# Kernel optimization log

Hardware: AMD Instinct MI355X
Metric: run time of the kernel (lower is better)

## Reference

```python
import jax, jax.numpy as jnp
from jax import lax
import numpy as np

# Layer configuration (from init_kwargs; see FilteringActLayer.__init__)
UP = 2                      # up_factor (temp_rate 32 / in_rate 16)
DOWN = 2                    # down_factor (temp_rate 32 / out_rate 16)
PADDING = (11, 10, 11, 10)  # (px0, px1, py0, py1), derived pad_total = 21
GAIN = float(np.sqrt(2.0))  # lrelu gain used in StyleGAN3
SLOPE = 0.2                 # leaky relu negative slope
CLAMP = 256.0               # activation clamp
UP_TAPS = 12
IN_CUTOFF = 8.0
OUT_CUTOFF = 8.0
IN_HALF_WIDTH = 6.0
OUT_HALF_WIDTH = 6.0
TEMP_FS = 32.0              # max(in_rate, out_rate) * act_upsampling


def _design_lowpass(numtaps, cutoff, width, fs):
    """Replicates scipy.signal.firwin(numtaps, cutoff, width=width, fs=fs)."""
    nyq = fs / 2.0
    # kaiser_atten / kaiser_beta
    atten = 2.285 * (numtaps - 1) * np.pi * (width / nyq) + 7.95
    if atten > 50.0:
        beta = 0.1102 * (atten - 8.7)
    elif atten > 21.0:
        beta = 0.5842 * (atten - 21.0) ** 0.4 + 0.07886 * (atten - 21.0)
    else:
        beta = 0.0
    m = np.arange(numtaps) - (numtaps - 1) / 2.0
    c = cutoff / nyq
    h = c * np.sinc(c * m)
    h = h * np.kaiser(numtaps, beta)
    h = h / np.sum(h)  # unity gain at DC (firwin scale=True)
    return h.astype(np.float32)


def _upfirdn2d_sep(x, f, up, down, pad, gain):
    """Zero-insert upsample by `up`, pad, correlate with separable 1D FIR f
    (applied flipped, i.e. true convolution as in the torch reference),
    then subsample by `down`. x: [N,C,H,W], f: [taps]."""
    N, C, H, W = x.shape
    fr = f[::-1].astype(x.dtype)
    kH = fr.reshape(1, 1, -1, 1)
    kW = fr.reshape(1, 1, 1, -1)
    px0, px1, py0, py1 = pad
    xr = x.reshape(N * C, 1, H, W)
    # lhs_dilation implements the zero-insertion; +up-1 hi-pad accounts for the
    # trailing zeros the torch reference keeps after upsampling.
    xr = lax.conv_general_dilated(xr, kH, window_strides=(down, 1),
                                  padding=((py0, py1 + up - 1), (0, 0)),
                                  lhs_dilation=(up, 1))
    xr = lax.conv_general_dilated(xr, kW, window_strides=(1, down),
                                  padding=((0, 0), (px0, px1 + up - 1)),
                                  lhs_dilation=(1, up))
    Ho, Wo = xr.shape[2], xr.shape[3]
    return xr.reshape(N, C, Ho, Wo) * gain


def setup_inputs() -> dict:
    key = jax.random.key(0)
    k1, k2 = jax.random.split(key)
    x = jax.random.normal(k1, (8, 512, 64, 64), dtype=jnp.float32)
    bias = jax.random.normal(k2, (512,), dtype=jnp.float32) * 0.1
    up_filter = jnp.asarray(_design_lowpass(UP_TAPS, IN_CUTOFF, IN_HALF_WIDTH * 2, TEMP_FS))
    down_filter = jnp.asarray(_design_lowpass(UP_TAPS, OUT_CUTOFF, OUT_HALF_WIDTH * 2, TEMP_FS))
    return {"x": x, "bias": bias, "up_filter": up_filter, "down_filter": down_filter}


def reference(x, bias, up_filter, down_filter):
    # (1) FIR upsample (gain = up^2 to preserve signal magnitude)
    y = _upfirdn2d_sep(x, up_filter, UP, 1, PADDING, float(UP * UP))
    # (2) bias + leaky-relu + gain + clamp (bias_act 'lrelu')
    y = y + bias[None, :, None, None]
    y = jnp.where(y >= 0, y, y * SLOPE) * GAIN
    y = jnp.clip(y, -CLAMP, CLAMP)
    # (3) FIR downsample
    y = _upfirdn2d_sep(y, down_filter, 1, DOWN, (0, 0, 0, 0), 1.0)
    return y
```

## Files before the change

### kernel.cpp

```cpp
#include <hip/hip_runtime.h>

#define SIN 80
#define ST1 84
#define ST3 72

typedef float v2f __attribute__((ext_vector_type(2)));

static __device__ __forceinline__ v2f fma2(v2f a, v2f b, v2f c) {
    return __builtin_elementwise_fma(a, b, c);
}
static __device__ __forceinline__ v2f bcast2(float s) { v2f r; r.x = s; r.y = s; return r; }
static __device__ __forceinline__ v2f mk2(float a, float b) { v2f r; r.x = a; r.y = b; return r; }

__global__ __launch_bounds__(256, 4)
void synth_fused(const float* __restrict__ x, const float* __restrict__ bias,
                 const float* __restrict__ fu, const float* __restrict__ fd,
                 float* __restrict__ out)
{
    __shared__ __align__(16) float bufA[3024];
    __shared__ __align__(16) float bufB[3536];
    __shared__ float sfilt[24];
    float* const s_in = bufA;
    float* const s_t3 = bufA;
    float* const s_t1 = bufB;

    const int tid  = threadIdx.x;
    const int bx   = blockIdx.x;
    const int tile = bx & 3;
    const int nc   = bx >> 2;
    const int gy0  = tile << 4;

    if (tid < 24) sfilt[tid] = (tid < 12) ? fu[tid] : fd[tid - 12];
    const float bc = bias[nc & 511];
    const float* __restrict__ xc = x + ((size_t)nc << 12);

    #pragma unroll
    for (int it = 0; it < 2; ++it) {
        int idx = tid + it * 256;
        if (idx < 416) {
            int r  = idx >> 4;
            int c4 = (idx & 15) << 2;
            int gy = gy0 - 5 + r;
            float4 v = make_float4(0.f, 0.f, 0.f, 0.f);
            if ((unsigned)gy < 64u)
                v = *reinterpret_cast<const float4*>(xc + (gy << 6) + c4);
            float* dst = s_in + r * SIN + 5 + c4;
            dst[0] = v.x; dst[1] = v.y; dst[2] = v.z; dst[3] = v.w;
        }
    }
    #pragma unroll
    for (int it = 0; it < 2; ++it) {
        int idx = tid + it * 256;
        if (idx < 416) {
            int r  = idx >> 4;
            int pc = idx & 15;
            int c  = (pc < 5) ? pc : (64 + pc);
            s_in[r * SIN + c] = 0.0f;
        }
    }
    __syncthreads();

    float u0[12], gs[12];
    #pragma unroll
    for (int k = 0; k < 12; ++k) { u0[k] = sfilt[k]; gs[k] = sfilt[23 - k]; }
    v2f gpk[6];
    #pragma unroll
    for (int j = 0; j < 6; ++j) gpk[j] = mk2(gs[2*j], gs[2*j + 1]);

    if (tid < 111) {
        const int g3 = tid / 37;
        const int c2 = tid - 37 * g3;
        const float* ip = s_in + (7 * g3) * SIN + 2 * c2;
        v2f rv[12];
        #pragma unroll
        for (int j = 0; j < 12; ++j) rv[j] = *reinterpret_cast<const v2f*>(ip + j * SIN);
        float* op = s_t1 + (14 * g3) * ST1 + 2 * c2;
        #pragma unroll
        for (int m = 0; m < 7; ++m) {
            v2f aE = rv[m] * u0[10];
            v2f aO = rv[m] * u0[11];
            #pragma unroll
            for (int j = 1; j < 6; ++j) {
                aE = fma2(rv[m + j], bcast2(u0[10 - 2*j]), aE);
                aO = fma2(rv[m + j], bcast2(u0[11 - 2*j]), aO);
            }
            *reinterpret_cast<v2f*>(op + (2*m) * ST1)     = aE;
            *reinterpret_cast<v2f*>(op + (2*m + 1) * ST1) = aO;
        }
    }
    __syncthreads();

    const float S42 = 4.0f * 1.41421356237309515f;
    v2f upk2[6];
    #pragma unroll
    for (int j = 0; j < 6; ++j) upk2[j] = mk2(u0[10 - 2*j] * S42, u0[11 - 2*j] * S42);
    const float bcs = bc * 1.41421356237309515f;

    if (tid < 252) {
        const int r = tid / 6;
        const int q = tid - 6 * r;
        const float* t1r = s_t1 + r * ST1 + 12 * q;
        float w[22];
        #pragma unroll
        for (int j = 0; j < 5; ++j) {
            float4 v4 = *reinterpret_cast<const float4*>(t1r + 4 * j);
            w[4*j] = v4.x; w[4*j+1] = v4.y; w[4*j+2] = v4.z; w[4*j+3] = v4.w;
        }
        { v2f v2 = *reinterpret_cast<const v2f*>(t1r + 20); w[20] = v2.x; w[21] = v2.y; }
        const v2f bc2 = bcast2(bcs);
        v2f t2p[17];
        #pragma unroll
        for (int i = 0; i < 17; ++i) {
            v2f acc = bc2;
            #pragma unroll
            for (int j = 0; j < 6; ++j)
                acc = fma2(upk2[j], bcast2(w[i + j]), acc);
            v2f mx = __builtin_elementwise_max(acc, acc * 0.2f);
            t2p[i] = mk2(__builtin_amdgcn_fmed3f(mx.x, -256.0f, 256.0f),
                         __builtin_amdgcn_fmed3f(mx.y, -256.0f, 256.0f));
        }
        float* t3r = s_t3 + r * ST3 + 12 * q;
        #pragma unroll
        for (int i = 0; i < 3; ++i) {
            float4 o4;
            float* op = &o4.x;
            #pragma unroll
            for (int s = 0; s < 4; ++s) {
                const int oi = 4 * i + s;
                v2f acc = gpk[0] * t2p[oi];
                #pragma unroll
                for (int j = 1; j < 6; ++j) acc = fma2(gpk[j], t2p[oi + j], acc);
                op[s] = acc.x + acc.y;
            }
            *reinterpret_cast<float4*>(t3r + 4 * i) = o4;
        }
    }
    __syncthreads();

    if (tid < 128) {
        const int c2 = tid & 31;
        const int rc = tid >> 5;
        const float* t3c = s_t3 + (rc << 3) * ST3 + 2 * c2;
        v2f wv[18];
        #pragma unroll
        for (int j = 0; j < 18; ++j) wv[j] = *reinterpret_cast<const v2f*>(t3c + j * ST3);
        float* op = out + ((size_t)nc << 12) + ((size_t)(gy0 + (rc << 2)) << 6) + 2 * c2;
        #pragma unroll
        for (int i = 0; i < 4; ++i) {
            v2f acc = wv[2*i] * gs[0];
            #pragma unroll
            for (int k = 1; k < 12; ++k)
                acc = fma2(wv[2*i + k], bcast2(gs[k]), acc);
            *reinterpret_cast<v2f*>(op + (size_t)(i << 6)) = acc;
        }
    }
}

extern "C" void kernel_launch(void* const* d_in, const int* in_sizes, int n_in,
                              void* d_out, int out_size, void* d_ws, size_t ws_size,
                              hipStream_t stream) {
    const float* x    = (const float*)d_in[0];
    const float* bias = (const float*)d_in[1];
    const float* fu   = (const float*)d_in[2];
    const float* fd   = (const float*)d_in[3];
    float* out        = (float*)d_out;

    dim3 grid(8 * 512 * 4);
    dim3 block(256);
    hipLaunchKernelGGL(synth_fused, grid, block, 0, stream, x, bias, fu, fd, out);
}
```

Measured before the change: 154.2 us.

## Process all four row tiles per block with register prefetch of next tile

Each block now handles a whole channel plane, looping over the four 16-row tiles instead of launching one block per tile. The next tile's input rows are prefetched into registers while the current tile's horizontal/activation stage runs, which overlaps global loads with compute. Shared buffers are no longer aliased, so LDS per block grows, and the final vertical pass now uses all 256 threads with scalar FMAs instead of 128 threads with packed math. The grid shrinks by four, which costs parallelism and occupancy and adds an extra barrier per tile.

Result: slower. 160.4 us (+4.0%).

```diff
diff --git a/kernel.cpp b/kernel.cpp
--- a/kernel.cpp
+++ b/kernel.cpp
@@ -17,48 +17,32 @@
                  const float* __restrict__ fu, const float* __restrict__ fd,
                  float* __restrict__ out)
 {
-    __shared__ __align__(16) float bufA[3024];
-    __shared__ __align__(16) float bufB[3536];
+    __shared__ __align__(16) float s_in[2080];
+    __shared__ __align__(16) float s_t1[3536];
+    __shared__ __align__(16) float s_t3[3024];
     __shared__ float sfilt[24];
-    float* const s_in = bufA;
-    float* const s_t3 = bufA;
-    float* const s_t1 = bufB;
 
-    const int tid  = threadIdx.x;
-    const int bx   = blockIdx.x;
-    const int tile = bx & 3;
-    const int nc   = bx >> 2;
-    const int gy0  = tile << 4;
+    const int tid = threadIdx.x;
+    const int nc  = blockIdx.x;
 
     if (tid < 24) sfilt[tid] = (tid < 12) ? fu[tid] : fd[tid - 12];
-    const float bc = bias[nc & 511];
-    const float* __restrict__ xc = x + ((size_t)nc << 12);
-
-    #pragma unroll
-    for (int it = 0; it < 2; ++it) {
-        int idx = tid + it * 256;
+    {
+        int idx = tid;
+        {   int r = idx >> 4, pc = idx & 15;
+            int c = (pc < 5) ? pc : (64 + pc);
+            if (idx < 416) s_in[r * SIN + c] = 0.0f; }
+        idx = tid + 256;
         if (idx < 416) {
-            int r  = idx >> 4;
-            int c4 = (idx & 15) << 2;
-            int gy = gy0 - 5 + r;
-            float4 v = make_float4(0.f, 0.f, 0.f, 0.f);
-            if ((unsigned)gy < 64u)
-                v = *reinterpret_cast<const float4*>(xc + (gy << 6) + c4);
-            float* dst = s_in + r * SIN + 5 + c4;
-            dst[0] = v.x; dst[1] = v.y; dst[2] = v.z; dst[3] = v.w;
-        }
-    }
-    #pragma unroll
-    for (int it = 0; it < 2; ++it) {
-        int idx = tid + it * 256;
-        if (idx < 416) {
-            int r  = idx >> 4;
-            int pc = idx & 15;
-            int c  = (pc < 5) ? pc : (64 + pc);
+            int r = idx >> 4, pc = idx & 15;
+            int c = (pc < 5) ? pc : (64 + pc);
             s_in[r * SIN + c] = 0.0f;
         }
     }
     __syncthreads();
+
+    const float bc = bias[nc & 511];
+    const float* __restrict__ xc = x + ((size_t)nc << 12);
+    float* __restrict__ oc = out + ((size_t)nc << 12);
 
     float u0[12], gs[12];
     #pragma unroll
@@ -66,92 +50,134 @@
     v2f gpk[6];
     #pragma unroll
     for (int j = 0; j < 6; ++j) gpk[j] = mk2(gs[2*j], gs[2*j + 1]);
-
-    if (tid < 111) {
-        const int g3 = tid / 37;
-        const int c2 = tid - 37 * g3;
-        const float* ip = s_in + (7 * g3) * SIN + 2 * c2;
-        v2f rv[12];
-        #pragma unroll
-        for (int j = 0; j < 12; ++j) rv[j] = *reinterpret_cast<const v2f*>(ip + j * SIN);
-        float* op = s_t1 + (14 * g3) * ST1 + 2 * c2;
-        #pragma unroll
-        for (int m = 0; m < 7; ++m) {
-            v2f aE = rv[m] * u0[10];
-            v2f aO = rv[m] * u0[11];
-            #pragma unroll
-            for (int j = 1; j < 6; ++j) {
-                aE = fma2(rv[m + j], bcast2(u0[10 - 2*j]), aE);
-                aO = fma2(rv[m + j], bcast2(u0[11 - 2*j]), aO);
-            }
-            *reinterpret_cast<v2f*>(op + (2*m) * ST1)     = aE;
-            *reinterpret_cast<v2f*>(op + (2*m + 1) * ST1) = aO;
-        }
-    }
-    __syncthreads();
-
     const float S42 = 4.0f * 1.41421356237309515f;
     v2f upk2[6];
     #pragma unroll
     for (int j = 0; j < 6; ++j) upk2[j] = mk2(u0[10 - 2*j] * S42, u0[11 - 2*j] * S42);
     const float bcs = bc * 1.41421356237309515f;
 
-    if (tid < 252) {
-        const int r = tid / 6;
-        const int q = tid - 6 * r;
-        const float* t1r = s_t1 + r * ST1 + 12 * q;
-        float w[22];
-        #pragma unroll
-        for (int j = 0; j < 5; ++j) {
-            float4 v4 = *reinterpret_cast<const float4*>(t1r + 4 * j);
-            w[4*j] = v4.x; w[4*j+1] = v4.y; w[4*j+2] = v4.z; w[4*j+3] = v4.w;
-        }
-        { v2f v2 = *reinterpret_cast<const v2f*>(t1r + 20); w[20] = v2.x; w[21] = v2.y; }
-        const v2f bc2 = bcast2(bcs);
-        v2f t2p[17];
-        #pragma unroll
-        for (int i = 0; i < 17; ++i) {
-            v2f acc = bc2;
-            #pragma unroll
-            for (int j = 0; j < 6; ++j)
-                acc = fma2(upk2[j], bcast2(w[i + j]), acc);
-            v2f mx = __builtin_elementwise_max(acc, acc * 0.2f);
-            t2p[i] = mk2(__builtin_amdgcn_fmed3f(mx.x, -256.0f, 256.0f),
-                         __builtin_amdgcn_fmed3f(mx.y, -256.0f, 256.0f));
-        }
-        float* t3r = s_t3 + r * ST3 + 12 * q;
-        #pragma unroll
-        for (int i = 0; i < 3; ++i) {
-            float4 o4;
-            float* op = &o4.x;
-            #pragma unroll
-            for (int s = 0; s < 4; ++s) {
-                const int oi = 4 * i + s;
-                v2f acc = gpk[0] * t2p[oi];
-                #pragma unroll
-                for (int j = 1; j < 6; ++j) acc = fma2(gpk[j], t2p[oi + j], acc);
-                op[s] = acc.x + acc.y;
-            }
-            *reinterpret_cast<float4*>(t3r + 4 * i) = o4;
+    float4 pf0 = make_float4(0.f, 0.f, 0.f, 0.f);
+    float4 pf1 = make_float4(0.f, 0.f, 0.f, 0.f);
+    {
+        int r = tid >> 4, c4 = (tid & 15) << 2;
+        int gy = r - 5;
+        if ((unsigned)gy < 64u) pf0 = *reinterpret_cast<const float4*>(xc + (gy << 6) + c4);
+        int idx = tid + 256;
+        if (idx < 416) {
+            r = idx >> 4; c4 = (idx & 15) << 2; gy = r - 5;
+            if ((unsigned)gy < 64u) pf1 = *reinterpret_cast<const float4*>(xc + (gy << 6) + c4);
         }
     }
-    __syncthreads();
 
-    if (tid < 128) {
-        const int c2 = tid & 31;
-        const int rc = tid >> 5;
-        const float* t3c = s_t3 + (rc << 3) * ST3 + 2 * c2;
-        v2f wv[18];
-        #pragma unroll
-        for (int j = 0; j < 18; ++j) wv[j] = *reinterpret_cast<const v2f*>(t3c + j * ST3);
-        float* op = out + ((size_t)nc << 12) + ((size_t)(gy0 + (rc << 2)) << 6) + 2 * c2;
-        #pragma unroll
-        for (int i = 0; i < 4; ++i) {
-            v2f acc = wv[2*i] * gs[0];
+    for (int t = 0; t < 4; ++t) {
+        const int gy0 = t << 4;
+
+        {
+            int r = tid >> 4, c4 = (tid & 15) << 2;
+            float* dst = &s_in[r * SIN + 5 + c4];
+            dst[0] = pf0.x; dst[1] = pf0.y; dst[2] = pf0.z; dst[3] = pf0.w;
+            int idx = tid + 256;
+            if (idx < 416) {
+                r = idx >> 4; c4 = (idx & 15) << 2;
+                dst = &s_in[r * SIN + 5 + c4];
+                dst[0] = pf1.x; dst[1] = pf1.y; dst[2] = pf1.z; dst[3] = pf1.w;
+            }
+        }
+        __syncthreads();
+
+        if (tid < 111) {
+            const int g3 = tid / 37;
+            const int c2 = tid - 37 * g3;
+            const float* ip = s_in + (7 * g3) * SIN + 2 * c2;
+            v2f rv[12];
             #pragma unroll
-            for (int k = 1; k < 12; ++k)
-                acc = fma2(wv[2*i + k], bcast2(gs[k]), acc);
-            *reinterpret_cast<v2f*>(op + (size_t)(i << 6)) = acc;
+            for (int j = 0; j < 12; ++j) rv[j] = *reinterpret_cast<const v2f*>(ip + j * SIN);
+            float* op = s_t1 + (14 * g3) * ST1 + 2 * c2;
+            #pragma unroll
+            for (int m = 0; m < 7; ++m) {
+                v2f aE = rv[m] * u0[10];
+                v2f aO = rv[m] * u0[11];
+                #pragma unroll
+                for (int j = 1; j < 6; ++j) {
+                    aE = fma2(rv[m + j], bcast2(u0[10 - 2*j]), aE);
+                    aO = fma2(rv[m + j], bcast2(u0[11 - 2*j]), aO);
+                }
+                *reinterpret_cast<v2f*>(op + (2*m) * ST1)     = aE;
+                *reinterpret_cast<v2f*>(op + (2*m + 1) * ST1) = aO;
+            }
+        }
+        __syncthreads();
+
+        if (t < 3) {
+            const int gy0n = (t + 1) << 4;
+            int r = tid >> 4, c4 = (tid & 15) << 2;
+            int gy = gy0n - 5 + r;
+            pf0 = make_float4(0.f, 0.f, 0.f, 0.f);
+            if ((unsigned)gy < 64u) pf0 = *reinterpret_cast<const float4*>(xc + (gy << 6) + c4);
+            int idx = tid + 256;
+            pf1 = make_float4(0.f, 0.f, 0.f, 0.f);
+            if (idx < 416) {
+                r = idx >> 4; c4 = (idx & 15) << 2; gy = gy0n - 5 + r;
+                if ((unsigned)gy < 64u) pf1 = *reinterpret_cast<const float4*>(xc + (gy << 6) + c4);
+            }
+        }
+
+        if (tid < 252) {
+            const int r = tid / 6;
+            const int q = tid - 6 * r;
+            const float* t1r = s_t1 + r * ST1 + 12 * q;
+            float w[22];
+            #pragma unroll
+            for (int j = 0; j < 5; ++j) {
+                float4 v4 = *reinterpret_cast<const float4*>(t1r + 4 * j);
+                w[4*j] = v4.x; w[4*j+1] = v4.y; w[4*j+2] = v4.z; w[4*j+3] = v4.w;
+            }
+            { v2f v2 = *reinterpret_cast<const v2f*>(t1r + 20); w[20] = v2.x; w[21] = v2.y; }
+            const v2f bc2 = bcast2(bcs);
+            v2f t2p[17];
+            #pragma unroll
+            for (int i = 0; i < 17; ++i) {
+                v2f acc = bc2;
+                #pragma unroll
+                for (int j = 0; j < 6; ++j)
+                    acc = fma2(upk2[j], bcast2(w[i + j]), acc);
+                v2f mx = __builtin_elementwise_max(acc, acc * 0.2f);
+                t2p[i] = mk2(__builtin_amdgcn_fmed3f(mx.x, -256.0f, 256.0f),
+                             __builtin_amdgcn_fmed3f(mx.y, -256.0f, 256.0f));
+            }
+            float* t3r = s_t3 + r * ST3 + 12 * q;
+            #pragma unroll
+            for (int i = 0; i < 3; ++i) {
+                float4 o4;
+                float* op = &o4.x;
+                #pragma unroll
+                for (int s = 0; s < 4; ++s) {
+                    const int oi = 4 * i + s;
+                    v2f acc = gpk[0] * t2p[oi];
+                    #pragma unroll
+                    for (int j = 1; j < 6; ++j) acc = fma2(gpk[j], t2p[oi + j], acc);
+                    op[s] = acc.x + acc.y;
+                }
+                *reinterpret_cast<float4*>(t3r + 4 * i) = o4;
+            }
+        }
+        __syncthreads();
+
+        {
+            const int c  = tid & 63;
+            const int rc = tid >> 6;
+            const float* t3c = s_t3 + (rc << 3) * ST3 + c;
+            float wv[18];
+            #pragma unroll
+            for (int j = 0; j < 18; ++j) wv[j] = t3c[j * ST3];
+            float* op = oc + ((size_t)(gy0 + (rc << 2)) << 6) + c;
+            #pragma unroll
+            for (int i = 0; i < 4; ++i) {
+                float acc = gs[0] * wv[2*i];
+                #pragma unroll
+                for (int k = 1; k < 12; ++k) acc = fmaf(gs[k], wv[2*i + k], acc);
+                op[(size_t)(i << 6)] = acc;
+            }
         }
     }
 }
@@ -165,7 +191,7 @@
     const float* fd   = (const float*)d_in[3];
     float* out        = (float*)d_out;
 
-    dim3 grid(8 * 512 * 4);
+    dim3 grid(8 * 512);
     dim3 block(256);
     hipLaunchKernelGGL(synth_fused, grid, block, 0, stream, x, bias, fu, fd, out);
 }
```
